# Kernel optimization log

Hardware: AMD Instinct MI355X
Metric: run time of the kernel (lower is better)

## Reference

```python
import jax, jax.numpy as jnp
import numpy as np

B, N, S, D1, D2 = 16, 4096, 1024, 128, 256
MLP = [256, 128]
BN_EPS = 1e-5


def setup_inputs() -> dict:
    key = jax.random.key(0)
    ks = jax.random.split(key, 12)
    inp = {
        "xyz1": jax.random.normal(ks[0], (B, 3, N), dtype=jnp.float32),
        "xyz2": jax.random.normal(ks[1], (B, 3, S), dtype=jnp.float32),
        "points1": jax.random.normal(ks[2], (B, D1, N), dtype=jnp.float32),
        "points2": jax.random.normal(ks[3], (B, D2, S), dtype=jnp.float32),
    }
    in_ch = D1 + D2  # 384
    chans = [in_ch] + MLP
    ki = 4
    for li in range(len(MLP)):
        cin, cout = chans[li], chans[li + 1]
        inp[f"w{li+1}"] = jax.random.normal(ks[ki], (cout, cin), dtype=jnp.float32) * (1.0 / np.sqrt(cin)); ki += 1
        inp[f"b{li+1}"] = jnp.zeros((cout,), dtype=jnp.float32)
        inp[f"g{li+1}"] = jnp.ones((cout,), dtype=jnp.float32)
        inp[f"beta{li+1}"] = jnp.zeros((cout,), dtype=jnp.float32)
    return inp


def _batchnorm1d(x, gamma, beta):
    # x: [B, C, N]; training-mode batch stats over (B, N)
    mean = jnp.mean(x, axis=(0, 2), keepdims=True)
    var = jnp.var(x, axis=(0, 2), keepdims=True)
    xhat = (x - mean) * jax.lax.rsqrt(var + BN_EPS)
    return xhat * gamma[None, :, None] + beta[None, :, None]


def reference(xyz1, xyz2, points1, points2, w1, b1, g1, beta1, w2, b2, g2, beta2):
    x1 = jnp.transpose(xyz1, (0, 2, 1))   # [B, N, 3]
    x2 = jnp.transpose(xyz2, (0, 2, 1))   # [B, S, 3]
    p2 = jnp.transpose(points2, (0, 2, 1))  # [B, S, D2]

    # squared pairwise distances [B, N, S]
    dists = jnp.sum((x1[:, :, None, :] - x2[:, None, :, :]) ** 2, axis=-1)
    # 3 smallest distances (original sorts then slices top-3)
    neg_d3, idx = jax.lax.top_k(-dists, 3)  # [B, N, 3]
    d3 = -neg_d3
    dist_recip = 1.0 / (d3 + 1e-8)
    weight = dist_recip / jnp.sum(dist_recip, axis=2, keepdims=True)  # [B, N, 3]

    # gather neighbor features: [B, N, 3, D2]
    feats = p2[jnp.arange(p2.shape[0])[:, None, None], idx]
    interp = jnp.sum(feats * weight[..., None], axis=2)  # [B, N, D2]

    p1 = jnp.transpose(points1, (0, 2, 1))  # [B, N, D1]
    new_points = jnp.concatenate([p1, interp], axis=-1)  # [B, N, D1+D2]
    x = jnp.transpose(new_points, (0, 2, 1))  # [B, C, N]

    for w, b, g, bt in ((w1, b1, g1, beta1), (w2, b2, g2, beta2)):
        x = jnp.einsum("oc,bcn->bon", w, x) + b[None, :, None]
        x = _batchnorm1d(x, g, bt)
        x = jax.nn.relu(x)
    return x
```

## Files before the change

### kernel.cpp

```cpp
#include <hip/hip_runtime.h>

typedef unsigned short u16;
typedef unsigned int   u32;
typedef unsigned long long u64;
typedef __attribute__((ext_vector_type(8))) short bf16x8;
typedef __attribute__((ext_vector_type(8))) unsigned short u16x8;
typedef __attribute__((ext_vector_type(4))) float f32x4;

#define NB   16
#define NPTS 4096
#define SPTS 1024
#define BNT  65536

#define G2L(src, dst) __builtin_amdgcn_global_load_lds( \
    (const __attribute__((address_space(1))) void*)(src), \
    (__attribute__((address_space(3))) void*)(dst), 16, 0, 0)

__device__ __forceinline__ float bf2f(u16 u){ return __uint_as_float(((u32)u)<<16); }
__device__ __forceinline__ u16 f2bf(float f){
  u32 u = __float_as_uint(f);
  return (u16)((u + 0x7FFFu + ((u>>16)&1u))>>16);
}

__global__ __launch_bounds__(256) void convw_k(const float* __restrict__ w1, const float* __restrict__ w2,
                                               u16* __restrict__ w1b, u16* __restrict__ w2b){
  int i = blockIdx.x*256 + threadIdx.x;
  if (i < 98304) w1b[i] = f2bf(w1[i]);
  else { int j = i - 98304; w2b[j] = f2bf(w2[j]); }
}

__global__ __launch_bounds__(256) void transpose_k(const float* __restrict__ in, u16* __restrict__ out,
                                                   int C, int S, int ostride){
  __shared__ float tl[64][65];
  int t = threadIdx.x;
  int b = blockIdx.y;
  int s0 = blockIdx.x * 64;
  for (int ct = 0; ct < C; ct += 64){
    __syncthreads();
    for (int i = t; i < 4096; i += 256){
      int sl = i & 63, cl = i >> 6;
      tl[sl][cl] = in[((size_t)b*C + ct + cl)*S + s0 + sl];
    }
    __syncthreads();
    for (int i = t; i < 4096; i += 256){
      int cl = i & 63, sl = i >> 6;
      out[((size_t)b*S + s0 + sl)*ostride + ct + cl] = f2bf(tl[sl][cl]);
    }
  }
}

__global__ __launch_bounds__(512) void knn_k(const float* __restrict__ xyz1, const float* __restrict__ xyz2,
                                             const u16* __restrict__ p2t, u16* __restrict__ X){
  __shared__ float4 sxyz[SPTS];
  __shared__ double pp[8][3][64];
  __shared__ float  swts[3][64];
  __shared__ int    sidx[3][64];
  int t  = threadIdx.x;
  int b  = blockIdx.x >> 6;
  int n0 = (blockIdx.x & 63) << 6;
  const float* x2b = xyz2 + (size_t)b*3*SPTS;
  for (int s = t; s < SPTS; s += 512)
    sxyz[s] = make_float4(x2b[s], x2b[SPTS+s], x2b[2*SPTS+s], 0.f);
  int q = t & 63, g = t >> 6;
  const float* x1b = xyz1 + (size_t)b*3*NPTS;
  int n = n0 + q;
  float qx = x1b[n], qy = x1b[NPTS+n], qz = x1b[2*NPTS+n];
  __syncthreads();

  double k0 = 1e300, k1 = 1e300, k2 = 1e300;
  int sBeg = g << 7;
  #pragma unroll 4
  for (int sj = 0; sj < 128; ++sj){
    int s = sBeg + sj;
    float4 p = sxyz[s];
    float dist;
    {
      #pragma clang fp contract(off)
      float dx = qx - p.x, dy = qy - p.y, dz = qz - p.z;
      dist = ((dx*dx) + (dy*dy)) + (dz*dz);
    }
    double pk = __longlong_as_double(__double_as_longlong((double)dist) | (long long)s);
    double n2 = fmin(fmax(pk, k1), k2);
    double n1 = fmin(fmax(pk, k0), k1);
    double n0d = fmin(pk, k0);
    k0 = n0d; k1 = n1; k2 = n2;
  }
  pp[g][0][q] = k0; pp[g][1][q] = k1; pp[g][2][q] = k2;
  __syncthreads();

  if (t < 64){
    double m0 = 1e300, m1 = 1e300, m2 = 1e300;
    #pragma unroll
    for (int gg = 0; gg < 8; ++gg){
      #pragma unroll
      for (int p = 0; p < 3; ++p){
        double pk = pp[gg][p][t];
        double n2 = fmin(fmax(pk, m1), m2);
        double n1 = fmin(fmax(pk, m0), m1);
        double n0d = fmin(pk, m0);
        m0 = n0d; m1 = n1; m2 = n2;
      }
    }
    int j0 = (int)(__double_as_longlong(m0) & 1023);
    int j1 = (int)(__double_as_longlong(m1) & 1023);
    int j2 = (int)(__double_as_longlong(m2) & 1023);
    float e0 = (float)m0, e1 = (float)m1, e2 = (float)m2;
    float r0 = 1.f/(e0 + 1e-8f), r1 = 1.f/(e1 + 1e-8f), r2 = 1.f/(e2 + 1e-8f);
    float rs = (r0 + r1) + r2;
    swts[0][t] = r0/rs; swts[1][t] = r1/rs; swts[2][t] = r2/rs;
    sidx[0][t] = j0;    sidx[1][t] = j1;    sidx[2][t] = j2;
  }
  __syncthreads();

  int w = t >> 6, lane = t & 63;
  for (int qq = w*8; qq < w*8 + 8; ++qq){
    float wa = swts[0][qq], wb = swts[1][qq], wc = swts[2][qq];
    int   j0 = sidx[0][qq], j1 = sidx[1][qq], j2 = sidx[2][qq];
    const ushort4 u0 = *(const ushort4*)(p2t + (((size_t)b*SPTS + j0)<<8) + (lane<<2));
    const ushort4 u1 = *(const ushort4*)(p2t + (((size_t)b*SPTS + j1)<<8) + (lane<<2));
    const ushort4 u2 = *(const ushort4*)(p2t + (((size_t)b*SPTS + j2)<<8) + (lane<<2));
    ushort4 ov;
    ov.x = f2bf(wa*bf2f(u0.x) + wb*bf2f(u1.x) + wc*bf2f(u2.x));
    ov.y = f2bf(wa*bf2f(u0.y) + wb*bf2f(u1.y) + wc*bf2f(u2.y));
    ov.z = f2bf(wa*bf2f(u0.z) + wb*bf2f(u1.z) + wc*bf2f(u2.z));
    ov.w = f2bf(wa*bf2f(u0.w) + wb*bf2f(u1.w) + wc*bf2f(u2.w));
    *(ushort4*)(X + ((size_t)b*NPTS + n0 + qq)*384 + 128 + (lane<<2)) = ov;
  }
}

__global__ __launch_bounds__(256) void gemm1_k(const u16* __restrict__ A, const u16* __restrict__ Bw,
                                               u16* __restrict__ Cc,
                                               float* __restrict__ psum, float* __restrict__ psq){
  const int K = 384, Nn = 256;
  __shared__ u16 lA[64*64];
  __shared__ u16 lB[256*64];
  float* sums = (float*)lA;
  float* sqs  = (float*)(lA + 512);
  int t = threadIdx.x, lane = t & 63, wid = t >> 6;
  int rowBase = blockIdx.x << 6;
  int wm = wid >> 1, wn = wid & 1;

  const char* pA[2]; int dAo[2];
  #pragma unroll
  for (int j = 0; j < 2; ++j){
    int L = j*4096 + t*16;
    int row = L >> 7, kb = L & 127;
    int kbs = kb ^ ((row & 7) << 4);
    pA[j] = (const char*)A + ((size_t)(rowBase + row)*K)*2 + kbs;
    dAo[j] = j*4096 + wid*1024;
  }
  const char* pB[8]; int dBo[8];
  #pragma unroll
  for (int j = 0; j < 8; ++j){
    int L = j*4096 + t*16;
    int row = L >> 7, kb = L & 127;
    int kbs = kb ^ ((row & 7) << 4);
    pB[j] = (const char*)Bw + ((size_t)row*K)*2 + kbs;
    dBo[j] = j*4096 + wid*1024;
  }

  f32x4 z = {0.f,0.f,0.f,0.f};
  f32x4 acc[2][8];
  #pragma unroll
  for (int m = 0; m < 2; ++m)
    #pragma unroll
    for (int n = 0; n < 8; ++n) acc[m][n] = z;

  #pragma unroll
  for (int kt = 0; kt < 6; ++kt){
    size_t ko = (size_t)kt * 128;
    #pragma unroll
    for (int j = 0; j < 2; ++j) G2L(pA[j] + ko, (char*)lA + dAo[j]);
    #pragma unroll
    for (int j = 0; j < 8; ++j) G2L(pB[j] + ko, (char*)lB + dBo[j]);
    __syncthreads();
    #pragma unroll
    for (int ks = 0; ks < 2; ++ks){
      bf16x8 af[2];
      #pragma unroll
      for (int m = 0; m < 2; ++m){
        int row = wm*32 + m*16 + (lane & 15);
        int sw = (row & 7) << 4;
        int kb = (ks*64 + ((lane >> 4) << 4)) ^ sw;
        af[m] = *(const bf16x8*)((const char*)lA + row*128 + kb);
      }
      #pragma unroll
      for (int n = 0; n < 8; ++n){
        int row = wn*128 + n*16 + (lane & 15);
        int sw = (row & 7) << 4;
        int kb = (ks*64 + ((lane >> 4) << 4)) ^ sw;
        bf16x8 bv = *(const bf16x8*)((const char*)lB + row*128 + kb);
        #pragma unroll
        for (int m = 0; m < 2; ++m)
          acc[m][n] = __builtin_amdgcn_mfma_f32_16x16x32_bf16(af[m], bv, acc[m][n], 0, 0, 0);
      }
    }
    __syncthreads();
  }

  sums[t] = 0.f; sqs[t] = 0.f;
  __syncthreads();
  int colb = wn*128 + (lane & 15);
  int rowb = rowBase + wm*32 + ((lane >> 4) << 2);
  #pragma unroll
  for (int n = 0; n < 8; ++n){
    float s = 0.f, qq2 = 0.f;
    #pragma unroll
    for (int m = 0; m < 2; ++m){
      #pragma unroll
      for (int r = 0; r < 4; ++r){
        float v = acc[m][n][r];
        Cc[(size_t)(rowb + m*16 + r)*Nn + colb + n*16] = f2bf(v);
        s += v; qq2 += v*v;
      }
    }
    atomicAdd(&sums[colb + n*16], s);
    atomicAdd(&sqs [colb + n*16], qq2);
  }
  __syncthreads();
  psum[(size_t)t*1024 + blockIdx.x] = sums[t];
  psq [(size_t)t*1024 + blockIdx.x] = sqs[t];
}

__global__ __launch_bounds__(256) void gemm2_k(const u16* __restrict__ A, const u16* __restrict__ Bw,
                                               u16* __restrict__ Cc,
                                               const float* __restrict__ sc, const float* __restrict__ sh,
                                               float* __restrict__ psum, float* __restrict__ psq){
  const int K = 256, Nn = 128;
  __shared__ u16 lA[64*64];
  __shared__ u16 lB[128*64];
  __shared__ float sums[128], sqs[128];
  int t = threadIdx.x, lane = t & 63, wid = t >> 6;
  int rowBase = blockIdx.x << 6;
  int wm = wid >> 1, wn = wid & 1;

  const char* pB[4]; int dBo[4];
  #pragma unroll
  for (int j = 0; j < 4; ++j){
    int L = j*4096 + t*16;
    int row = L >> 7, kb = L & 127;
    int kbs = kb ^ ((row & 7) << 4);
    pB[j] = (const char*)Bw + ((size_t)row*K)*2 + kbs;
    dBo[j] = j*4096 + wid*1024;
  }
  int arow = t & 63, achunk = t >> 6;
  const u16* pArow = A + (size_t)(rowBase + arow)*K + achunk*16;
  int asw = (arow & 7) << 4;
  char* wA0 = (char*)lA + arow*128 + ((achunk*32)      ^ asw);
  char* wA1 = (char*)lA + arow*128 + ((achunk*32 + 16) ^ asw);

  f32x4 z = {0.f,0.f,0.f,0.f};
  f32x4 acc[2][4];
  #pragma unroll
  for (int m = 0; m < 2; ++m)
    #pragma unroll
    for (int n = 0; n < 4; ++n) acc[m][n] = z;

  for (int kk = 0; kk < K; kk += 64){
    size_t ko = (size_t)kk * 2;
    #pragma unroll
    for (int j = 0; j < 4; ++j) G2L(pB[j] + ko, (char*)lB + dBo[j]);
    u16x8 y0 = *(const u16x8*)(pArow + kk);
    u16x8 y1 = *(const u16x8*)(pArow + kk + 8);
    int k0 = kk + achunk*16;
    bf16x8 o0, o1;
    #pragma unroll
    for (int j = 0; j < 8; ++j){
      float v = bf2f((u16)y0[j]) * sc[k0 + j] + sh[k0 + j];
      o0[j] = (short)f2bf(fmaxf(v, 0.f));
    }
    #pragma unroll
    for (int j = 0; j < 8; ++j){
      float v = bf2f((u16)y1[j]) * sc[k0 + 8 + j] + sh[k0 + 8 + j];
      o1[j] = (short)f2bf(fmaxf(v, 0.f));
    }
    *(bf16x8*)wA0 = o0;
    *(bf16x8*)wA1 = o1;
    __syncthreads();
    bf16x8 af[2][2], bfv[4][2];
    #pragma unroll
    for (int m = 0; m < 2; ++m){
      int row = wm*32 + m*16 + (lane & 15);
      int sw = (row & 7) << 4;
      #pragma unroll
      for (int ks = 0; ks < 2; ++ks){
        int kb = (ks*64 + ((lane >> 4) << 4)) ^ sw;
        af[m][ks] = *(const bf16x8*)((const char*)lA + row*128 + kb);
      }
    }
    #pragma unroll
    for (int n = 0; n < 4; ++n){
      int row = wn*64 + n*16 + (lane & 15);
      int sw = (row & 7) << 4;
      #pragma unroll
      for (int ks = 0; ks < 2; ++ks){
        int kb = (ks*64 + ((lane >> 4) << 4)) ^ sw;
        bfv[n][ks] = *(const bf16x8*)((const char*)lB + row*128 + kb);
      }
    }
    #pragma unroll
    for (int ks = 0; ks < 2; ++ks)
      #pragma unroll
      for (int m = 0; m < 2; ++m)
        #pragma unroll
        for (int n = 0; n < 4; ++n)
          acc[m][n] = __builtin_amdgcn_mfma_f32_16x16x32_bf16(af[m][ks], bfv[n][ks], acc[m][n], 0, 0, 0);
    __syncthreads();
  }

  if (t < 128){ sums[t] = 0.f; sqs[t] = 0.f; }
  __syncthreads();
  int colb = wn*64 + (lane & 15);
  int rowb = rowBase + wm*32 + ((lane >> 4) << 2);
  #pragma unroll
  for (int n = 0; n < 4; ++n){
    float s = 0.f, qq2 = 0.f;
    #pragma unroll
    for (int m = 0; m < 2; ++m){
      #pragma unroll
      for (int r = 0; r < 4; ++r){
        float v = acc[m][n][r];
        Cc[(size_t)(rowb + m*16 + r)*Nn + colb + n*16] = f2bf(v);
        s += v; qq2 += v*v;
      }
    }
    atomicAdd(&sums[colb + n*16], s);
    atomicAdd(&sqs [colb + n*16], qq2);
  }
  __syncthreads();
  if (t < 128){
    psum[(size_t)t*1024 + blockIdx.x] = sums[t];
    psq [(size_t)t*1024 + blockIdx.x] = sqs[t];
  }
}

__global__ __launch_bounds__(256) void finalize2_k(const float* __restrict__ psum, const float* __restrict__ psq,
                                                   const float* __restrict__ g, const float* __restrict__ bet,
                                                   float* __restrict__ sc, float* __restrict__ sh){
  __shared__ float rs[256], rq[256];
  int c = blockIdx.x, t = threadIdx.x;
  float s = 0.f, q = 0.f;
  for (int rt = t; rt < 1024; rt += 256){
    s += psum[(size_t)c*1024 + rt];
    q += psq [(size_t)c*1024 + rt];
  }
  rs[t] = s; rq[t] = q;
  __syncthreads();
  for (int off = 128; off; off >>= 1){
    if (t < off){ rs[t] += rs[t+off]; rq[t] += rq[t+off]; }
    __syncthreads();
  }
  if (t == 0){
    const float inv = 1.f/65536.f;
    float mean = rs[0]*inv;
    float var  = rq[0]*inv - mean*mean;
    float rstd = rsqrtf(var + 1e-5f);
    float scl  = g[c]*rstd;
    sc[c] = scl;
    sh[c] = bet[c] - mean*scl;
  }
}

__global__ __launch_bounds__(256) void finalout_k(const u16* __restrict__ y2, const float* __restrict__ sc,
                                                  const float* __restrict__ sh, float* __restrict__ out){
  __shared__ float tl[128][65];
  int t  = threadIdx.x;
  int b  = blockIdx.x >> 6;
  int n0 = (blockIdx.x & 63) << 6;
  for (int i = t; i < 8192; i += 256){
    int r = i >> 7, c = i & 127;
    float v = bf2f(y2[((size_t)b*NPTS + n0 + r)*128 + c]);
    v = fmaxf(v*sc[c] + sh[c], 0.f);
    tl[c][r] = v;
  }
  __syncthreads();
  for (int i = t; i < 8192; i += 256){
    int o = i >> 6, j = i & 63;
    out[(size_t)b*128*NPTS + (size_t)o*NPTS + n0 + j] = tl[o][j];
  }
}

extern "C" void kernel_launch(void* const* d_in, const int* in_sizes, int n_in,
                              void* d_out, int out_size, void* d_ws, size_t ws_size,
                              hipStream_t stream) {
  const float* xyz1    = (const float*)d_in[0];
  const float* xyz2    = (const float*)d_in[1];
  const float* points1 = (const float*)d_in[2];
  const float* points2 = (const float*)d_in[3];
  const float* w1      = (const float*)d_in[4];
  const float* g1      = (const float*)d_in[6];
  const float* beta1   = (const float*)d_in[7];
  const float* w2      = (const float*)d_in[8];
  const float* g2      = (const float*)d_in[10];
  const float* beta2   = (const float*)d_in[11];

  char* ws = (char*)d_ws;
  u16*  X    = (u16*)ws;
  u16*  Y2   = (u16*)ws;
  u16*  Y1   = (u16*)(ws + 50331648);
  u16*  p2t  = (u16*)(ws + 83886080);
  u16*  w1b  = (u16*)(ws + 92274688);
  u16*  w2b  = (u16*)(ws + 92471296);
  float* psum1 = (float*)(ws + 83886080);
  float* psq1  = (float*)(ws + 84934656);
  float* psum2 = (float*)(ws + 85983232);
  float* psq2  = (float*)(ws + 86507520);
  float* sc1   = (float*)(ws + 87031808);
  float* sh1   = (float*)(ws + 87032832);
  float* sc2   = (float*)(ws + 87033856);
  float* sh2   = (float*)(ws + 87034368);

  convw_k<<<512, 256, 0, stream>>>(w1, w2, w1b, w2b);
  transpose_k<<<dim3(64, 16), 256, 0, stream>>>(points1, X,   128, NPTS, 384);
  transpose_k<<<dim3(16, 16), 256, 0, stream>>>(points2, p2t, 256, SPTS, 256);
  knn_k<<<1024, 512, 0, stream>>>(xyz1, xyz2, p2t, X);
  gemm1_k<<<1024, 256, 0, stream>>>(X, w1b, Y1, psum1, psq1);
  finalize2_k<<<256, 256, 0, stream>>>(psum1, psq1, g1, beta1, sc1, sh1);
  gemm2_k<<<1024, 256, 0, stream>>>(Y1, w2b, Y2, sc1, sh1, psum2, psq2);
  finalize2_k<<<128, 256, 0, stream>>>(psum2, psq2, g2, beta2, sc2, sh2);
  finalout_k<<<1024, 256, 0, stream>>>(Y2, sc2, sh2, (float*)d_out);
}
```

Before: 153.5 us.

## Halve KNN block size, stage GEMM1 output in LDS, transpose partial-stat layout

KNN blocks now handle 32 queries with 16 groups each scanning 64 candidates, doubling the grid to raise parallelism. GEMM1 writes its bf16 tile into LDS first and then stores coalesced 16-byte rows to global memory, instead of scattered 2-byte stores. It also reduces the column sums with wave shuffles before the LDS atomics, so fewer atomics are issued. Partial statistics are stored block-major, and finalize now handles 8 channels per block with contiguous reads. The cost is more LDS traffic and an extra barrier in GEMM1, plus a longer merge in KNN.

```diff
diff --git a/kernel.cpp b/kernel.cpp
--- a/kernel.cpp
+++ b/kernel.cpp
@@ -2,7 +2,6 @@
 
 typedef unsigned short u16;
 typedef unsigned int   u32;
-typedef unsigned long long u64;
 typedef __attribute__((ext_vector_type(8))) short bf16x8;
 typedef __attribute__((ext_vector_type(8))) unsigned short u16x8;
 typedef __attribute__((ext_vector_type(4))) float f32x4;
@@ -52,25 +51,25 @@
 __global__ __launch_bounds__(512) void knn_k(const float* __restrict__ xyz1, const float* __restrict__ xyz2,
                                              const u16* __restrict__ p2t, u16* __restrict__ X){
   __shared__ float4 sxyz[SPTS];
-  __shared__ double pp[8][3][64];
-  __shared__ float  swts[3][64];
-  __shared__ int    sidx[3][64];
+  __shared__ double pp[16][3][32];
+  __shared__ float  swts[3][32];
+  __shared__ int    sidx[3][32];
   int t  = threadIdx.x;
-  int b  = blockIdx.x >> 6;
-  int n0 = (blockIdx.x & 63) << 6;
+  int b  = blockIdx.x >> 7;
+  int n0 = (blockIdx.x & 127) << 5;
   const float* x2b = xyz2 + (size_t)b*3*SPTS;
   for (int s = t; s < SPTS; s += 512)
     sxyz[s] = make_float4(x2b[s], x2b[SPTS+s], x2b[2*SPTS+s], 0.f);
-  int q = t & 63, g = t >> 6;
+  int q = t & 31, g = t >> 5;
   const float* x1b = xyz1 + (size_t)b*3*NPTS;
   int n = n0 + q;
   float qx = x1b[n], qy = x1b[NPTS+n], qz = x1b[2*NPTS+n];
   __syncthreads();
 
   double k0 = 1e300, k1 = 1e300, k2 = 1e300;
-  int sBeg = g << 7;
+  int sBeg = g << 6;
   #pragma unroll 4
-  for (int sj = 0; sj < 128; ++sj){
+  for (int sj = 0; sj < 64; ++sj){
     int s = sBeg + sj;
     float4 p = sxyz[s];
     float dist;
@@ -88,10 +87,10 @@
   pp[g][0][q] = k0; pp[g][1][q] = k1; pp[g][2][q] = k2;
   __syncthreads();
 
-  if (t < 64){
+  if (t < 32){
     double m0 = 1e300, m1 = 1e300, m2 = 1e300;
     #pragma unroll
-    for (int gg = 0; gg < 8; ++gg){
+    for (int gg = 0; gg < 16; ++gg){
       #pragma unroll
       for (int p = 0; p < 3; ++p){
         double pk = pp[gg][p][t];
@@ -113,7 +112,7 @@
   __syncthreads();
 
   int w = t >> 6, lane = t & 63;
-  for (int qq = w*8; qq < w*8 + 8; ++qq){
+  for (int qq = w*4; qq < w*4 + 4; ++qq){
     float wa = swts[0][qq], wb = swts[1][qq], wc = swts[2][qq];
     int   j0 = sidx[0][qq], j1 = sidx[1][qq], j2 = sidx[2][qq];
     const ushort4 u0 = *(const ushort4*)(p2t + (((size_t)b*SPTS + j0)<<8) + (lane<<2));
@@ -131,11 +130,11 @@
 __global__ __launch_bounds__(256) void gemm1_k(const u16* __restrict__ A, const u16* __restrict__ Bw,
                                                u16* __restrict__ Cc,
                                                float* __restrict__ psum, float* __restrict__ psq){
-  const int K = 384, Nn = 256;
+  const int K = 384;
   __shared__ u16 lA[64*64];
   __shared__ u16 lB[256*64];
   float* sums = (float*)lA;
-  float* sqs  = (float*)(lA + 512);
+  float* sqs  = sums + 256;
   int t = threadIdx.x, lane = t & 63, wid = t >> 6;
   int rowBase = blockIdx.x << 6;
   int wm = wid >> 1, wn = wid & 1;
@@ -146,7 +145,7 @@
     int L = j*4096 + t*16;
     int row = L >> 7, kb = L & 127;
     int kbs = kb ^ ((row & 7) << 4);
-    pA[j] = (const char*)A + ((size_t)(rowBase + row)*K)*2 + kbs;
+    pA[j] = (const char*)A + (size_t)(rowBase + row)*768 + kbs;
     dAo[j] = j*4096 + wid*1024;
   }
   const char* pB[8]; int dBo[8];
@@ -155,7 +154,7 @@
     int L = j*4096 + t*16;
     int row = L >> 7, kb = L & 127;
     int kbs = kb ^ ((row & 7) << 4);
-    pB[j] = (const char*)Bw + ((size_t)row*K)*2 + kbs;
+    pB[j] = (const char*)Bw + (size_t)row*768 + kbs;
     dBo[j] = j*4096 + wid*1024;
   }
 
@@ -190,9 +189,8 @@
         int sw = (row & 7) << 4;
         int kb = (ks*64 + ((lane >> 4) << 4)) ^ sw;
         bf16x8 bv = *(const bf16x8*)((const char*)lB + row*128 + kb);
-        #pragma unroll
-        for (int m = 0; m < 2; ++m)
-          acc[m][n] = __builtin_amdgcn_mfma_f32_16x16x32_bf16(af[m], bv, acc[m][n], 0, 0, 0);
+        acc[0][n] = __builtin_amdgcn_mfma_f32_16x16x32_bf16(af[0], bv, acc[0][n], 0, 0, 0);
+        acc[1][n] = __builtin_amdgcn_mfma_f32_16x16x32_bf16(af[1], bv, acc[1][n], 0, 0, 0);
       }
     }
     __syncthreads();
@@ -200,26 +198,35 @@
 
   sums[t] = 0.f; sqs[t] = 0.f;
   __syncthreads();
+  u16* bb = lB;
   int colb = wn*128 + (lane & 15);
-  int rowb = rowBase + wm*32 + ((lane >> 4) << 2);
+  int rowb_l = wm*32 + ((lane >> 4) << 2);
   #pragma unroll
   for (int n = 0; n < 8; ++n){
-    float s = 0.f, qq2 = 0.f;
+    float s = 0.f, q = 0.f;
     #pragma unroll
     for (int m = 0; m < 2; ++m){
       #pragma unroll
       for (int r = 0; r < 4; ++r){
         float v = acc[m][n][r];
-        Cc[(size_t)(rowb + m*16 + r)*Nn + colb + n*16] = f2bf(v);
-        s += v; qq2 += v*v;
-      }
-    }
-    atomicAdd(&sums[colb + n*16], s);
-    atomicAdd(&sqs [colb + n*16], qq2);
-  }
-  __syncthreads();
-  psum[(size_t)t*1024 + blockIdx.x] = sums[t];
-  psq [(size_t)t*1024 + blockIdx.x] = sqs[t];
+        bb[(rowb_l + m*16 + r)*256 + colb + n*16] = f2bf(v);
+        s += v; q += v*v;
+      }
+    }
+    s += __shfl_xor(s, 16); s += __shfl_xor(s, 32);
+    q += __shfl_xor(q, 16); q += __shfl_xor(q, 32);
+    if (lane < 16){
+      atomicAdd(&sums[colb + n*16], s);
+      atomicAdd(&sqs [colb + n*16], q);
+    }
+  }
+  __syncthreads();
+  psum[(size_t)blockIdx.x*256 + t] = sums[t];
+  psq [(size_t)blockIdx.x*256 + t] = sqs[t];
+  u16* dst = Cc + (size_t)rowBase*256;
+  #pragma unroll
+  for (int i = 0; i < 8; ++i)
+    *(u16x8*)(dst + i*2048 + t*8) = *(const u16x8*)(bb + i*2048 + t*8);
 }
 
 __global__ __launch_bounds__(256) void gemm2_k(const u16* __restrict__ A, const u16* __restrict__ Bw,
@@ -329,31 +336,41 @@
   }
   __syncthreads();
   if (t < 128){
-    psum[(size_t)t*1024 + blockIdx.x] = sums[t];
-    psq [(size_t)t*1024 + blockIdx.x] = sqs[t];
+    psum[(size_t)blockIdx.x*128 + t] = sums[t];
+    psq [(size_t)blockIdx.x*128 + t] = sqs[t];
   }
 }
 
 __global__ __launch_bounds__(256) void finalize2_k(const float* __restrict__ psum, const float* __restrict__ psq,
                                                    const float* __restrict__ g, const float* __restrict__ bet,
-                                                   float* __restrict__ sc, float* __restrict__ sh){
-  __shared__ float rs[256], rq[256];
-  int c = blockIdx.x, t = threadIdx.x;
-  float s = 0.f, q = 0.f;
-  for (int rt = t; rt < 1024; rt += 256){
-    s += psum[(size_t)c*1024 + rt];
-    q += psq [(size_t)c*1024 + rt];
-  }
-  rs[t] = s; rq[t] = q;
+                                                   float* __restrict__ sc, float* __restrict__ sh,
+                                                   int C, int NBLK){
+  __shared__ float ls[256][8], lq[256][8];
+  int c0 = blockIdx.x*8, t = threadIdx.x;
+  float s[8], q[8];
+  #pragma unroll
+  for (int j = 0; j < 8; ++j){ s[j] = 0.f; q[j] = 0.f; }
+  for (int rb = t; rb < NBLK; rb += 256){
+    const float* ps = psum + (size_t)rb*C + c0;
+    const float* pq = psq  + (size_t)rb*C + c0;
+    #pragma unroll
+    for (int j = 0; j < 8; ++j){ s[j] += ps[j]; q[j] += pq[j]; }
+  }
+  #pragma unroll
+  for (int j = 0; j < 8; ++j){ ls[t][j] = s[j]; lq[t][j] = q[j]; }
   __syncthreads();
   for (int off = 128; off; off >>= 1){
-    if (t < off){ rs[t] += rs[t+off]; rq[t] += rq[t+off]; }
-    __syncthreads();
-  }
-  if (t == 0){
+    if (t < off){
+      #pragma unroll
+      for (int j = 0; j < 8; ++j){ ls[t][j] += ls[t+off][j]; lq[t][j] += lq[t+off][j]; }
+    }
+    __syncthreads();
+  }
+  if (t < 8){
+    int c = c0 + t;
     const float inv = 1.f/65536.f;
-    float mean = rs[0]*inv;
-    float var  = rq[0]*inv - mean*mean;
+    float mean = ls[0][t]*inv;
+    float var  = lq[0][t]*inv - mean*mean;
     float rstd = rsqrtf(var + 1e-5f);
     float scl  = g[c]*rstd;
     sc[c] = scl;
@@ -413,10 +430,10 @@
   convw_k<<<512, 256, 0, stream>>>(w1, w2, w1b, w2b);
   transpose_k<<<dim3(64, 16), 256, 0, stream>>>(points1, X,   128, NPTS, 384);
   transpose_k<<<dim3(16, 16), 256, 0, stream>>>(points2, p2t, 256, SPTS, 256);
-  knn_k<<<1024, 512, 0, stream>>>(xyz1, xyz2, p2t, X);
+  knn_k<<<2048, 512, 0, stream>>>(xyz1, xyz2, p2t, X);
   gemm1_k<<<1024, 256, 0, stream>>>(X, w1b, Y1, psum1, psq1);
-  finalize2_k<<<256, 256, 0, stream>>>(psum1, psq1, g1, beta1, sc1, sh1);
+  finalize2_k<<<32, 256, 0, stream>>>(psum1, psq1, g1, beta1, sc1, sh1, 256, 1024);
   gemm2_k<<<1024, 256, 0, stream>>>(Y1, w2b, Y2, sc1, sh1, psum2, psq2);
-  finalize2_k<<<128, 256, 0, stream>>>(psum2, psq2, g2, beta2, sc2, sh2);
+  finalize2_k<<<16, 256, 0, stream>>>(psum2, psq2, g2, beta2, sc2, sh2, 128, 1024);
   finalout_k<<<1024, 256, 0, stream>>>(Y2, sc2, sh2, (float*)d_out);
 }
```

Result: faster. 148.8 us (-3.1%).
